# Kernel tuning notes

Measured on AMD Instinct MI355X. Metric: run time of the kernel, lower is better.

## Reference

```python
import jax, jax.numpy as jnp
import numpy as np
from jax import lax

L, H, NUM_CONVS, KSIZE = 8192, 128, 4, 7
EPS = 1e-5


def _pos_encoding(length, dim, dtype):
    pos = jnp.arange(length, dtype=jnp.float32)[:, None]
    i = jnp.arange(dim, dtype=jnp.float32)[None, :]
    angle = pos / jnp.power(10000.0, (2.0 * jnp.floor(i / 2.0)) / dim)
    pe = jnp.where((jnp.arange(dim) % 2 == 0)[None, :], jnp.sin(angle), jnp.cos(angle))
    return pe.astype(dtype)


def _layer_norm(x):
    mu = jnp.mean(x, axis=-1, keepdims=True)
    var = jnp.mean(jnp.square(x - mu), axis=-1, keepdims=True)
    return (x - mu) * lax.rsqrt(var + EPS)


def _conv1d_same(x, w, b):
    # x: [L, H]; w: [H_out, H_in, K]; b: [H_out]. SAME padding over sequence.
    lhs = x.T[None]  # [1, H, L]
    out = lax.conv_general_dilated(lhs, w, window_strides=(1,), padding='SAME',
                                   dimension_numbers=('NCH', 'OIH', 'NCH'))
    return (out[0] + b[:, None]).T  # [L, H]


def setup_inputs() -> dict:
    key = jax.random.key(0)
    ks = jax.random.split(key, 12)
    s = 0.02
    return {
        'x': jax.random.normal(ks[0], (L, H), jnp.float32),
        'conv_w': jax.random.normal(ks[1], (NUM_CONVS, H, H, KSIZE), jnp.float32) * s,
        'conv_b': jax.random.normal(ks[2], (NUM_CONVS, H), jnp.float32) * s,
        'Wq': jax.random.normal(ks[3], (H, H), jnp.float32) * s,
        'bq': jax.random.normal(ks[4], (H,), jnp.float32) * s,
        'Wk': jax.random.normal(ks[5], (H, H), jnp.float32) * s,
        'bk': jax.random.normal(ks[6], (H,), jnp.float32) * s,
        'Wv': jax.random.normal(ks[7], (H, H), jnp.float32) * s,
        'bv': jax.random.normal(ks[8], (H,), jnp.float32) * s,
        'Wff': jax.random.normal(ks[9], (H, H), jnp.float32) * s,
        'bff': jax.random.normal(ks[10], (H,), jnp.float32) * s,
    }


def reference(x, conv_w, conv_b, Wq, bq, Wk, bk, Wv, bv, Wff, bff):
    h = x + _pos_encoding(x.shape[0], x.shape[1], x.dtype)
    # conv stack: LN -> conv -> residual, repeated num_convs times
    for i in range(NUM_CONVS):
        residual = h
        h = _conv1d_same(_layer_norm(h), conv_w[i], conv_b[i]) + residual
    # self-attention (single-head as written in the source)
    residual = h
    n = _layer_norm(h)
    q = n @ Wq.T + bq
    k = n @ Wk.T + bk
    v = n @ Wv.T + bv
    scale = 1.0 / jnp.sqrt(jnp.asarray(H, h.dtype))
    attn = jax.nn.softmax((q @ k.T) * scale, axis=-1)  # [L, L]
    h = attn @ v + residual
    # feed-forward
    residual = h
    h = jax.nn.relu(_layer_norm(h) @ Wff.T + bff) + residual
    return h
```

## Files before the change

### kernel.cpp

```cpp
#include <hip/hip_runtime.h>

#define LL 8192
#define HH 128

typedef __attribute__((ext_vector_type(8))) short short8v;
typedef __attribute__((ext_vector_type(4))) short short4v;
typedef __attribute__((ext_vector_type(4))) float f32x4;

__device__ inline short f2bf(float f) {
    union { float f; unsigned u; } x; x.f = f;
    unsigned r = (x.u + 0x7fffu + ((x.u >> 16) & 1u)) >> 16;
    return (short)r;
}
__device__ inline float bf2f(short s) {
    union { unsigned u; float f; } x; x.u = ((unsigned)(unsigned short)s) << 16;
    return x.f;
}

__global__ __launch_bounds__(256) void repack_conv_wb(const float* __restrict__ w,
                                                      short* __restrict__ wkb) {
    int idx = blockIdx.x * 256 + threadIdx.x;
    int k = idx % 7;
    int t = idx / 7;
    int i = t % HH; t /= HH;
    int o = t % HH;
    int lay = t / HH;
    wkb[((lay * 7 + k) * HH + o) * HH + i] = f2bf(w[idx]);
}

__global__ __launch_bounds__(256) void repack_qkv_wb(const float* __restrict__ Wq,
                                                     const float* __restrict__ Wk,
                                                     const float* __restrict__ Wv,
                                                     const float* __restrict__ bq,
                                                     const float* __restrict__ bk,
                                                     const float* __restrict__ bv,
                                                     short* __restrict__ wqkvb,
                                                     float* __restrict__ b3) {
    const float qs = 0.08838834764831845f;
    int idx = blockIdx.x * 256 + threadIdx.x;
    if (idx < 3 * 16384) {
        int t = idx >> 14, r = idx & 16383;
        float v = (t == 0) ? Wq[r] * qs : (t == 1) ? Wk[r] : Wv[r];
        wqkvb[idx] = f2bf(v);
    } else if (idx < 3 * 16384 + 384) {
        int j = idx - 3 * 16384;
        b3[j] = (j < 128) ? bq[j] * qs : (j < 256) ? bk[j - 128] : bv[j - 256];
    }
}

__global__ __launch_bounds__(256) void repack_ff_wb(const float* __restrict__ Wff,
                                                    short* __restrict__ wffb) {
    int idx = blockIdx.x * 256 + threadIdx.x;
    wffb[idx] = f2bf(Wff[idx]);
}

template <bool POS>
__global__ __launch_bounds__(256) void conv_ln_kernel(const float* __restrict__ hin,
                                                      const short* __restrict__ wkb,
                                                      const float* __restrict__ bias,
                                                      float* __restrict__ hout) {
    __shared__ float sF[22][132];
    __shared__ short sA[22][136];
    int tid = threadIdx.x;
    int w = tid >> 6, lane = tid & 63;
    int l15 = lane & 15, quad = lane >> 4;
    int m0 = blockIdx.x * 16;

    for (int idx = tid; idx < 22 * 32; idx += 256) {
        int r = idx >> 5, c4 = (idx & 31) << 2;
        int gl = m0 - 3 + r;
        float4 val = make_float4(0.f, 0.f, 0.f, 0.f);
        if (gl >= 0 && gl < LL) {
            val = *(const float4*)&hin[gl * HH + c4];
            if (POS) {
#pragma unroll
                for (int j = 0; j < 4; j++) {
                    int i = c4 + j;
                    float e = (float)(i & ~1) / 128.f;
                    float ang = (float)gl / powf(10000.f, e);
                    float pe = (i & 1) ? cosf(ang) : sinf(ang);
                    ((float*)&val)[j] += pe;
                }
            }
        }
        *(float4*)&sF[r][c4] = val;
    }
    __syncthreads();
#pragma unroll
    for (int rr = 0; rr < 6; rr++) {
        int row = rr * 4 + w;
        if (row < 22) {
            float2 xv = *(const float2*)&sF[row][lane * 2];
            float s = xv.x + xv.y, s2 = xv.x * xv.x + xv.y * xv.y;
#pragma unroll
            for (int off = 32; off >= 1; off >>= 1) {
                s  += __shfl_xor(s,  off, 64);
                s2 += __shfl_xor(s2, off, 64);
            }
            float mu = s * (1.f / 128.f);
            float var = s2 * (1.f / 128.f) - mu * mu;
            float rstd = rsqrtf(var + 1e-5f);
            unsigned lo = (unsigned short)f2bf((xv.x - mu) * rstd);
            unsigned hi = (unsigned short)f2bf((xv.y - mu) * rstd);
            ((unsigned*)&sA[row][0])[lane] = lo | (hi << 16);
        }
    }
    __syncthreads();
    int c0 = w * 32;
    f32x4 acc0 = (f32x4)(0.f), acc1 = (f32x4)(0.f);
    for (int k = 0; k < 7; k++) {
        const short* b0 = wkb + (k * HH + c0 + l15) * HH;
        const short* b1 = b0 + 16 * HH;
#pragma unroll
        for (int ks = 0; ks < 4; ks++) {
            short8v af = *(const short8v*)&sA[l15 + k][ks * 32 + quad * 8];
            short8v bf0 = *(const short8v*)&b0[ks * 32 + quad * 8];
            short8v bf1 = *(const short8v*)&b1[ks * 32 + quad * 8];
            acc0 = __builtin_amdgcn_mfma_f32_16x16x32_bf16(af, bf0, acc0, 0, 0, 0);
            acc1 = __builtin_amdgcn_mfma_f32_16x16x32_bf16(af, bf1, acc1, 0, 0, 0);
        }
    }
    float bb0 = bias[c0 + l15], bb1 = bias[c0 + 16 + l15];
#pragma unroll
    for (int r = 0; r < 4; r++) {
        int lr = quad * 4 + r;
        hout[(m0 + lr) * HH + c0 + l15]      = sF[lr + 3][c0 + l15]      + acc0[r] + bb0;
        hout[(m0 + lr) * HH + c0 + 16 + l15] = sF[lr + 3][c0 + 16 + l15] + acc1[r] + bb1;
    }
}

__global__ __launch_bounds__(256) void qkv_kernel(const float* __restrict__ hin,
                                                  const short* __restrict__ wqkvb,
                                                  const float* __restrict__ b3,
                                                  short* __restrict__ qb,
                                                  short* __restrict__ kb,
                                                  short* __restrict__ vt) {
    __shared__ float sF[16][132];
    __shared__ short sA[16][136];
    __shared__ short sT[4][32][17];
    int tid = threadIdx.x;
    int w = tid >> 6, lane = tid & 63;
    int l15 = lane & 15, quad = lane >> 4;
    int m0 = blockIdx.x * 16;

    for (int idx = tid; idx < 16 * 32; idx += 256) {
        int r = idx >> 5, c4 = (idx & 31) << 2;
        *(float4*)&sF[r][c4] = *(const float4*)&hin[(m0 + r) * HH + c4];
    }
    __syncthreads();
#pragma unroll
    for (int rr = 0; rr < 4; rr++) {
        int row = rr * 4 + w;
        float2 xv = *(const float2*)&sF[row][lane * 2];
        float s = xv.x + xv.y, s2 = xv.x * xv.x + xv.y * xv.y;
#pragma unroll
        for (int off = 32; off >= 1; off >>= 1) {
            s  += __shfl_xor(s,  off, 64);
            s2 += __shfl_xor(s2, off, 64);
        }
        float mu = s * (1.f / 128.f);
        float var = s2 * (1.f / 128.f) - mu * mu;
        float rstd = rsqrtf(var + 1e-5f);
        unsigned lo = (unsigned short)f2bf((xv.x - mu) * rstd);
        unsigned hi = (unsigned short)f2bf((xv.y - mu) * rstd);
        ((unsigned*)&sA[row][0])[lane] = lo | (hi << 16);
    }
    __syncthreads();

    short8v af[4];
#pragma unroll
    for (int ks = 0; ks < 4; ks++)
        af[ks] = *(const short8v*)&sA[l15][ks * 32 + quad * 8];
    int c0 = w * 32;

    for (int t = 0; t < 3; t++) {
        f32x4 acc0 = (f32x4)(0.f), acc1 = (f32x4)(0.f);
        const short* b0 = wqkvb + (t * 128 + c0 + l15) * HH;
        const short* b1 = b0 + 16 * HH;
#pragma unroll
        for (int ks = 0; ks < 4; ks++) {
            short8v bf0 = *(const short8v*)&b0[ks * 32 + quad * 8];
            short8v bf1 = *(const short8v*)&b1[ks * 32 + quad * 8];
            acc0 = __builtin_amdgcn_mfma_f32_16x16x32_bf16(af[ks], bf0, acc0, 0, 0, 0);
            acc1 = __builtin_amdgcn_mfma_f32_16x16x32_bf16(af[ks], bf1, acc1, 0, 0, 0);
        }
        float bb0 = b3[t * 128 + c0 + l15], bb1 = b3[t * 128 + c0 + 16 + l15];
        if (t < 2) {
            short* o = (t == 0) ? qb : kb;
#pragma unroll
            for (int r = 0; r < 4; r++) {
                int lr = m0 + quad * 4 + r;
                o[lr * HH + c0 + l15]      = f2bf(acc0[r] + bb0);
                o[lr * HH + c0 + 16 + l15] = f2bf(acc1[r] + bb1);
            }
        } else {
#pragma unroll
            for (int r = 0; r < 4; r++) {
                sT[w][l15][quad * 4 + r]      = f2bf(acc0[r] + bb0);
                sT[w][16 + l15][quad * 4 + r] = f2bf(acc1[r] + bb1);
            }
            asm volatile("s_waitcnt lgkmcnt(0)" ::: "memory");
#pragma unroll
            for (int cc = 0; cc < 8; cc++) {
                int col = cc * 4 + quad;
                vt[(c0 + col) * LL + m0 + l15] = sT[w][col][l15];
            }
        }
    }
}

#define NSPLIT 8
#define SEGROWS (LL / NSPLIT)
#define FBN 64

__global__ __launch_bounds__(256, 2) void flash_mfma_kernel(const short* __restrict__ qs,
                                                            const short* __restrict__ ksrc,
                                                            const short* __restrict__ vsrc,
                                                            short* __restrict__ PO,
                                                            float* __restrict__ Pl) {
    __shared__ short sK[16 * 64 * 8];
    __shared__ short sV[16 * 64 * 8];
    __shared__ short sP[4][32][88];

    const int tid = threadIdx.x;
    const int w = tid >> 6, lane = tid & 63;
    const int l15 = lane & 15, quad = lane >> 4;
    const int m0 = blockIdx.x * 128;
    const int seg = blockIdx.y;
    const int jbeg = seg * SEGROWS;

    const int knt_base = 0;
    const int vdt_base = (w >> 1);
    const int vks2 = w & 1;

    short8v qf[2][4];
#pragma unroll
    for (int mt = 0; mt < 2; mt++)
#pragma unroll
        for (int ks = 0; ks < 4; ks++)
            qf[mt][ks] = *(const short8v*)&qs[(m0 + w * 32 + mt * 16 + l15) * HH + ks * 32 + quad * 8];

    float l_r[2][4] = {{0.f, 0.f, 0.f, 0.f}, {0.f, 0.f, 0.f, 0.f}};
    f32x4 o_acc[2][8];
#pragma unroll
    for (int mt = 0; mt < 2; mt++)
#pragma unroll
        for (int dt = 0; dt < 8; dt++) o_acc[mt][dt] = (f32x4)(0.f);

    short8v kr[4], vr[4];
#pragma unroll
    for (int r = 0; r < 4; r++) {
        kr[r] = *(const short8v*)&ksrc[(jbeg + r * 16 + l15) * HH + w * 32 + quad * 8];
        vr[r] = *(const short8v*)&vsrc[((2 * r + vdt_base) * 16 + l15) * LL + jbeg + vks2 * 32 + quad * 8];
    }

    for (int c = 0; c < SEGROWS / FBN; c++) {
        const int j0 = jbeg + c * FBN;
        __syncthreads();
#pragma unroll
        for (int r = 0; r < 4; r++) {
            *(short8v*)&sK[((w + 4 * r) * 64 + lane) * 8] = kr[r];
            *(short8v*)&sV[((w + 4 * r) * 64 + lane) * 8] = vr[r];
        }
        __syncthreads();
        if (c + 1 < SEGROWS / FBN) {
            const int j1 = j0 + FBN;
#pragma unroll
            for (int r = 0; r < 4; r++) {
                kr[r] = *(const short8v*)&ksrc[(j1 + r * 16 + l15) * HH + w * 32 + quad * 8];
                vr[r] = *(const short8v*)&vsrc[((2 * r + vdt_base) * 16 + l15) * LL + j1 + vks2 * 32 + quad * 8];
            }
        }
        f32x4 s_acc[2][4];
#pragma unroll
        for (int mt = 0; mt < 2; mt++)
#pragma unroll
            for (int nt = 0; nt < 4; nt++) s_acc[mt][nt] = (f32x4)(0.f);
#pragma unroll
        for (int nt = 0; nt < 4; nt++)
#pragma unroll
            for (int ks = 0; ks < 4; ks++) {
                short8v kf = *(const short8v*)&sK[((nt * 4 + ks) * 64 + lane) * 8];
                s_acc[0][nt] = __builtin_amdgcn_mfma_f32_16x16x32_bf16(qf[0][ks], kf, s_acc[0][nt], 0, 0, 0);
                s_acc[1][nt] = __builtin_amdgcn_mfma_f32_16x16x32_bf16(qf[1][ks], kf, s_acc[1][nt], 0, 0, 0);
            }
#pragma unroll
        for (int mt = 0; mt < 2; mt++)
#pragma unroll
            for (int nt = 0; nt < 4; nt++)
#pragma unroll
                for (int r = 0; r < 4; r++) {
                    float p = __expf(fminf(s_acc[mt][nt][r], 30.f));
                    l_r[mt][r] += p;
                    sP[w][mt * 16 + quad * 4 + r][nt * 16 + l15] = f2bf(p);
                }
        asm volatile("s_waitcnt lgkmcnt(0)" ::: "memory");
#pragma unroll
        for (int ks2 = 0; ks2 < 2; ks2++) {
            short8v pf0 = *(const short8v*)&sP[w][l15][ks2 * 32 + quad * 8];
            short8v pf1 = *(const short8v*)&sP[w][16 + l15][ks2 * 32 + quad * 8];
#pragma unroll
            for (int dt = 0; dt < 8; dt++) {
                short8v vf = *(const short8v*)&sV[((dt * 2 + ks2) * 64 + lane) * 8];
                o_acc[0][dt] = __builtin_amdgcn_mfma_f32_16x16x32_bf16(pf0, vf, o_acc[0][dt], 0, 0, 0);
                o_acc[1][dt] = __builtin_amdgcn_mfma_f32_16x16x32_bf16(pf1, vf, o_acc[1][dt], 0, 0, 0);
            }
        }
    }
#pragma unroll
    for (int mt = 0; mt < 2; mt++)
#pragma unroll
        for (int r = 0; r < 4; r++) {
            float v = l_r[mt][r];
            v += __shfl_xor(v, 1, 64);
            v += __shfl_xor(v, 2, 64);
            v += __shfl_xor(v, 4, 64);
            v += __shfl_xor(v, 8, 64);
            if (l15 == 0)
                Pl[seg * LL + m0 + w * 32 + mt * 16 + quad * 4 + r] = v;
        }
#pragma unroll
    for (int mt = 0; mt < 2; mt++)
#pragma unroll
        for (int dt = 0; dt < 8; dt++)
#pragma unroll
            for (int r = 0; r < 4; r++)
                PO[(size_t)seg * LL * HH + (m0 + w * 32 + mt * 16 + quad * 4 + r) * HH + dt * 16 + l15] =
                    f2bf(o_acc[mt][dt][r]);
}

__global__ __launch_bounds__(256) void ff_kernel(const float* __restrict__ hin,
                                                 const short* __restrict__ PO,
                                                 const float* __restrict__ Pl,
                                                 const short* __restrict__ wffb,
                                                 const float* __restrict__ bff,
                                                 float* __restrict__ out) {
    __shared__ float sF[16][132];
    __shared__ short sA[16][136];
    __shared__ float sLi[16];
    int tid = threadIdx.x;
    int w = tid >> 6, lane = tid & 63;
    int l15 = lane & 15, quad = lane >> 4;
    int m0 = blockIdx.x * 16;

    if (tid < 16) {
        float s = 0.f;
#pragma unroll
        for (int seg = 0; seg < NSPLIT; seg++) s += Pl[seg * LL + m0 + tid];
        sLi[tid] = 1.f / s;
    }
    __syncthreads();
    for (int idx = tid; idx < 16 * 32; idx += 256) {
        int r = idx >> 5, c4 = (idx & 31) << 2;
        float4 hv = *(const float4*)&hin[(m0 + r) * HH + c4];
        float s0 = 0.f, s1 = 0.f, s2 = 0.f, s3 = 0.f;
#pragma unroll
        for (int seg = 0; seg < NSPLIT; seg++) {
            short4v pv = *(const short4v*)&PO[(size_t)seg * LL * HH + (m0 + r) * HH + c4];
            s0 += bf2f(pv[0]); s1 += bf2f(pv[1]); s2 += bf2f(pv[2]); s3 += bf2f(pv[3]);
        }
        float li = sLi[r];
        float4 val = make_float4(hv.x + s0 * li, hv.y + s1 * li, hv.z + s2 * li, hv.w + s3 * li);
        *(float4*)&sF[r][c4] = val;
    }
    __syncthreads();
#pragma unroll
    for (int rr = 0; rr < 4; rr++) {
        int row = rr * 4 + w;
        float2 xv = *(const float2*)&sF[row][lane * 2];
        float s = xv.x + xv.y, s2 = xv.x * xv.x + xv.y * xv.y;
#pragma unroll
        for (int off = 32; off >= 1; off >>= 1) {
            s  += __shfl_xor(s,  off, 64);
            s2 += __shfl_xor(s2, off, 64);
        }
        float mu = s * (1.f / 128.f);
        float var = s2 * (1.f / 128.f) - mu * mu;
        float rstd = rsqrtf(var + 1e-5f);
        unsigned lo = (unsigned short)f2bf((xv.x - mu) * rstd);
        unsigned hi = (unsigned short)f2bf((xv.y - mu) * rstd);
        ((unsigned*)&sA[row][0])[lane] = lo | (hi << 16);
    }
    __syncthreads();
    int c0 = w * 32;
    f32x4 acc0 = (f32x4)(0.f), acc1 = (f32x4)(0.f);
    const short* b0 = wffb + (c0 + l15) * HH;
    const short* b1 = b0 + 16 * HH;
#pragma unroll
    for (int ks = 0; ks < 4; ks++) {
        short8v af = *(const short8v*)&sA[l15][ks * 32 + quad * 8];
        short8v bf0 = *(const short8v*)&b0[ks * 32 + quad * 8];
        short8v bf1 = *(const short8v*)&b1[ks * 32 + quad * 8];
        acc0 = __builtin_amdgcn_mfma_f32_16x16x32_bf16(af, bf0, acc0, 0, 0, 0);
        acc1 = __builtin_amdgcn_mfma_f32_16x16x32_bf16(af, bf1, acc1, 0, 0, 0);
    }
    float bb0 = bff[c0 + l15], bb1 = bff[c0 + 16 + l15];
#pragma unroll
    for (int r = 0; r < 4; r++) {
        int lr = quad * 4 + r;
        float z0 = fmaxf(acc0[r] + bb0, 0.f) + sF[lr][c0 + l15];
        float z1 = fmaxf(acc1[r] + bb1, 0.f) + sF[lr][c0 + 16 + l15];
        out[(m0 + lr) * HH + c0 + l15]      = z0;
        out[(m0 + lr) * HH + c0 + 16 + l15] = z1;
    }
}

extern "C" void kernel_launch(void* const* d_in, const int* in_sizes, int n_in,
                              void* d_out, int out_size, void* d_ws, size_t ws_size,
                              hipStream_t stream) {
    const float* x      = (const float*)d_in[0];
    const float* conv_w = (const float*)d_in[1];
    const float* conv_b = (const float*)d_in[2];
    const float* Wq = (const float*)d_in[3];
    const float* bq = (const float*)d_in[4];
    const float* Wk = (const float*)d_in[5];
    const float* bk = (const float*)d_in[6];
    const float* Wv = (const float*)d_in[7];
    const float* bv = (const float*)d_in[8];
    const float* Wff = (const float*)d_in[9];
    const float* bff = (const float*)d_in[10];
    float* out = (float*)d_out;

    char* ws = (char*)d_ws;
    const size_t MB = 1u << 20;
    float* hB    = (float*)(ws);
    short* qb    = (short*)(ws + 4 * MB);
    short* kb    = (short*)(ws + 6 * MB);
    short* vt    = (short*)(ws + 8 * MB);
    float* Pl    = (float*)(ws + 10 * MB);
    short* wffb  = (short*)(ws + 10 * MB + 262144);
    float* b3    = (float*)(ws + 10 * MB + 294912);
    short* PO    = (short*)(ws + 10 * MB + 524288);
    float* hA    = (float*)(ws + 10 * MB + 524288);
    short* wkb   = (short*)(ws + 14 * MB + 524288);
    short* wqkvb = (short*)(ws + 15 * MB + 524288);

    repack_conv_wb<<<1792, 256, 0, stream>>>(conv_w, wkb);
    repack_qkv_wb<<<194, 256, 0, stream>>>(Wq, Wk, Wv, bq, bk, bv, wqkvb, b3);
    repack_ff_wb<<<64, 256, 0, stream>>>(Wff, wffb);

    const int KW = 7 * HH * HH;
    conv_ln_kernel<true ><<<LL / 16, 256, 0, stream>>>(x,  wkb + 0 * KW, conv_b + 0 * HH, hA);
    conv_ln_kernel<false><<<LL / 16, 256, 0, stream>>>(hA, wkb + 1 * KW, conv_b + 1 * HH, hB);
    conv_ln_kernel<false><<<LL / 16, 256, 0, stream>>>(hB, wkb + 2 * KW, conv_b + 2 * HH, hA);
    conv_ln_kernel<false><<<LL / 16, 256, 0, stream>>>(hA, wkb + 3 * KW, conv_b + 3 * HH, hB);

    qkv_kernel<<<LL / 16, 256, 0, stream>>>(hB, wqkvb, b3, qb, kb, vt);

    flash_mfma_kernel<<<dim3(LL / 128, NSPLIT), 256, 0, stream>>>(qb, kb, vt, PO, Pl);

    ff_kernel<<<LL / 16, 256, 0, stream>>>(hB, PO, Pl, wffb, bff, out);
}
```

Measured before the change: 222.0 us.

## Fuse four conv layers and QKV into one halo-recompute kernel, widen attention split

All four LayerNorm+conv residual layers and the QKV projection now run in one kernel. Each block keeps a 48-row window (16 output rows plus 16-row halos) in shared memory across layers, so the intermediate activations no longer round-trip through global memory between launches. The price is about three times the conv MFMA work per output row. The three weight-repack kernels are merged into one launch. When the workspace is large enough, the flash-attention KV split goes from 8 to 16 segments, and P is converted to bf16 by truncation instead of round-to-nearest, which slightly changes numerics.

```diff
diff --git a/kernel.cpp b/kernel.cpp
--- a/kernel.cpp
+++ b/kernel.cpp
@@ -17,161 +17,155 @@
     return x.f;
 }
 
-__global__ __launch_bounds__(256) void repack_conv_wb(const float* __restrict__ w,
-                                                      short* __restrict__ wkb) {
-    int idx = blockIdx.x * 256 + threadIdx.x;
-    int k = idx % 7;
-    int t = idx / 7;
-    int i = t % HH; t /= HH;
-    int o = t % HH;
-    int lay = t / HH;
-    wkb[((lay * 7 + k) * HH + o) * HH + i] = f2bf(w[idx]);
-}
-
-__global__ __launch_bounds__(256) void repack_qkv_wb(const float* __restrict__ Wq,
-                                                     const float* __restrict__ Wk,
-                                                     const float* __restrict__ Wv,
-                                                     const float* __restrict__ bq,
-                                                     const float* __restrict__ bk,
-                                                     const float* __restrict__ bv,
-                                                     short* __restrict__ wqkvb,
-                                                     float* __restrict__ b3) {
+__device__ inline unsigned ln_pack(const float* rowF, int lane) {
+    float2 xv = *(const float2*)&rowF[lane * 2];
+    float s = xv.x + xv.y, s2 = xv.x * xv.x + xv.y * xv.y;
+#pragma unroll
+    for (int off = 32; off >= 1; off >>= 1) {
+        s  += __shfl_xor(s,  off, 64);
+        s2 += __shfl_xor(s2, off, 64);
+    }
+    float mu = s * (1.f / 128.f);
+    float var = s2 * (1.f / 128.f) - mu * mu;
+    float rstd = rsqrtf(var + 1e-5f);
+    unsigned lo = (unsigned short)f2bf((xv.x - mu) * rstd);
+    unsigned hi = (unsigned short)f2bf((xv.y - mu) * rstd);
+    return lo | (hi << 16);
+}
+
+__global__ __launch_bounds__(256) void repack_all(const float* __restrict__ w,
+                                                  const float* __restrict__ Wq,
+                                                  const float* __restrict__ Wk,
+                                                  const float* __restrict__ Wv,
+                                                  const float* __restrict__ bq,
+                                                  const float* __restrict__ bk,
+                                                  const float* __restrict__ bv,
+                                                  const float* __restrict__ Wff,
+                                                  short* __restrict__ wkb,
+                                                  short* __restrict__ wqkvb,
+                                                  float* __restrict__ b3,
+                                                  short* __restrict__ wffb) {
     const float qs = 0.08838834764831845f;
     int idx = blockIdx.x * 256 + threadIdx.x;
-    if (idx < 3 * 16384) {
-        int t = idx >> 14, r = idx & 16383;
-        float v = (t == 0) ? Wq[r] * qs : (t == 1) ? Wk[r] : Wv[r];
-        wqkvb[idx] = f2bf(v);
-    } else if (idx < 3 * 16384 + 384) {
-        int j = idx - 3 * 16384;
-        b3[j] = (j < 128) ? bq[j] * qs : (j < 256) ? bk[j - 128] : bv[j - 256];
-    }
-}
-
-__global__ __launch_bounds__(256) void repack_ff_wb(const float* __restrict__ Wff,
-                                                    short* __restrict__ wffb) {
-    int idx = blockIdx.x * 256 + threadIdx.x;
-    wffb[idx] = f2bf(Wff[idx]);
-}
-
-template <bool POS>
-__global__ __launch_bounds__(256) void conv_ln_kernel(const float* __restrict__ hin,
-                                                      const short* __restrict__ wkb,
-                                                      const float* __restrict__ bias,
-                                                      float* __restrict__ hout) {
-    __shared__ float sF[22][132];
-    __shared__ short sA[22][136];
-    int tid = threadIdx.x;
-    int w = tid >> 6, lane = tid & 63;
-    int l15 = lane & 15, quad = lane >> 4;
-    int m0 = blockIdx.x * 16;
-
-    for (int idx = tid; idx < 22 * 32; idx += 256) {
-        int r = idx >> 5, c4 = (idx & 31) << 2;
-        int gl = m0 - 3 + r;
-        float4 val = make_float4(0.f, 0.f, 0.f, 0.f);
-        if (gl >= 0 && gl < LL) {
-            val = *(const float4*)&hin[gl * HH + c4];
-            if (POS) {
-#pragma unroll
-                for (int j = 0; j < 4; j++) {
-                    int i = c4 + j;
-                    float e = (float)(i & ~1) / 128.f;
-                    float ang = (float)gl / powf(10000.f, e);
-                    float pe = (i & 1) ? cosf(ang) : sinf(ang);
-                    ((float*)&val)[j] += pe;
-                }
-            }
-        }
-        *(float4*)&sF[r][c4] = val;
-    }
-    __syncthreads();
-#pragma unroll
-    for (int rr = 0; rr < 6; rr++) {
-        int row = rr * 4 + w;
-        if (row < 22) {
-            float2 xv = *(const float2*)&sF[row][lane * 2];
-            float s = xv.x + xv.y, s2 = xv.x * xv.x + xv.y * xv.y;
-#pragma unroll
-            for (int off = 32; off >= 1; off >>= 1) {
-                s  += __shfl_xor(s,  off, 64);
-                s2 += __shfl_xor(s2, off, 64);
-            }
-            float mu = s * (1.f / 128.f);
-            float var = s2 * (1.f / 128.f) - mu * mu;
-            float rstd = rsqrtf(var + 1e-5f);
-            unsigned lo = (unsigned short)f2bf((xv.x - mu) * rstd);
-            unsigned hi = (unsigned short)f2bf((xv.y - mu) * rstd);
-            ((unsigned*)&sA[row][0])[lane] = lo | (hi << 16);
-        }
-    }
-    __syncthreads();
-    int c0 = w * 32;
-    f32x4 acc0 = (f32x4)(0.f), acc1 = (f32x4)(0.f);
-    for (int k = 0; k < 7; k++) {
-        const short* b0 = wkb + (k * HH + c0 + l15) * HH;
-        const short* b1 = b0 + 16 * HH;
-#pragma unroll
-        for (int ks = 0; ks < 4; ks++) {
-            short8v af = *(const short8v*)&sA[l15 + k][ks * 32 + quad * 8];
-            short8v bf0 = *(const short8v*)&b0[ks * 32 + quad * 8];
-            short8v bf1 = *(const short8v*)&b1[ks * 32 + quad * 8];
-            acc0 = __builtin_amdgcn_mfma_f32_16x16x32_bf16(af, bf0, acc0, 0, 0, 0);
-            acc1 = __builtin_amdgcn_mfma_f32_16x16x32_bf16(af, bf1, acc1, 0, 0, 0);
-        }
-    }
-    float bb0 = bias[c0 + l15], bb1 = bias[c0 + 16 + l15];
-#pragma unroll
-    for (int r = 0; r < 4; r++) {
-        int lr = quad * 4 + r;
-        hout[(m0 + lr) * HH + c0 + l15]      = sF[lr + 3][c0 + l15]      + acc0[r] + bb0;
-        hout[(m0 + lr) * HH + c0 + 16 + l15] = sF[lr + 3][c0 + 16 + l15] + acc1[r] + bb1;
-    }
-}
-
-__global__ __launch_bounds__(256) void qkv_kernel(const float* __restrict__ hin,
-                                                  const short* __restrict__ wqkvb,
-                                                  const float* __restrict__ b3,
-                                                  short* __restrict__ qb,
-                                                  short* __restrict__ kb,
-                                                  short* __restrict__ vt) {
-    __shared__ float sF[16][132];
-    __shared__ short sA[16][136];
+    if (idx < 458752) {
+        int k = idx % 7;
+        int t = idx / 7;
+        int i = t % HH; t /= HH;
+        int o = t % HH;
+        int lay = t / HH;
+        wkb[((lay * 7 + k) * HH + o) * HH + i] = f2bf(w[idx]);
+    } else {
+        int j = idx - 458752;
+        if (j < 49152) {
+            int t = j >> 14, r = j & 16383;
+            float v = (t == 0) ? Wq[r] * qs : (t == 1) ? Wk[r] : Wv[r];
+            wqkvb[j] = f2bf(v);
+        } else if (j < 49536) {
+            int jj = j - 49152;
+            b3[jj] = (jj < 128) ? bq[jj] * qs : (jj < 256) ? bk[jj - 128] : bv[jj - 256];
+        } else if (j < 65920) {
+            int jj = j - 49536;
+            wffb[jj] = f2bf(Wff[jj]);
+        }
+    }
+}
+
+__global__ __launch_bounds__(256) void conv4qkv_kernel(const float* __restrict__ x,
+                                                       const short* __restrict__ wkb,
+                                                       const float* __restrict__ conv_b,
+                                                       const short* __restrict__ wqkvb,
+                                                       const float* __restrict__ b3,
+                                                       float* __restrict__ hB,
+                                                       short* __restrict__ qb,
+                                                       short* __restrict__ kb,
+                                                       short* __restrict__ vt) {
+    __shared__ float sF[48][132];
+    __shared__ short sA[54][136];
     __shared__ short sT[4][32][17];
     int tid = threadIdx.x;
     int w = tid >> 6, lane = tid & 63;
     int l15 = lane & 15, quad = lane >> 4;
     int m0 = blockIdx.x * 16;
-
+    int c0 = w * 32;
+
+    for (int idx = tid; idx < 48 * 32; idx += 256) {
+        int r = idx >> 5, c4 = (idx & 31) << 2;
+        int g = m0 - 16 + r;
+        float4 val = make_float4(0.f, 0.f, 0.f, 0.f);
+        if (g >= 0 && g < LL) {
+            val = *(const float4*)&x[g * HH + c4];
+#pragma unroll
+            for (int j = 0; j < 4; j++) {
+                int i = c4 + j;
+                float e = (float)(i & ~1) / 128.f;
+                float ang = (float)g / powf(10000.f, e);
+                float pe = (i & 1) ? cosf(ang) : sinf(ang);
+                ((float*)&val)[j] += pe;
+            }
+        }
+        *(float4*)&sF[r][c4] = val;
+    }
+    for (int idx = tid; idx < 6 * 68; idx += 256) {
+        int rr = idx / 68, cc = idx % 68;
+        int row = (rr < 3) ? rr : 48 + rr;
+        ((unsigned*)&sA[row][0])[cc] = 0u;
+    }
+
+    for (int lay = 0; lay < 4; lay++) {
+        __syncthreads();
+#pragma unroll
+        for (int rr = 0; rr < 12; rr++) {
+            int row = rr * 4 + w;
+            int g = m0 - 16 + row;
+            unsigned packed = ln_pack(&sF[row][0], lane);
+            if (g < 0 || g >= LL) packed = 0u;
+            ((unsigned*)&sA[row + 3][0])[lane] = packed;
+        }
+        __syncthreads();
+        f32x4 acc[3][2];
+#pragma unroll
+        for (int mt = 0; mt < 3; mt++) { acc[mt][0] = (f32x4)(0.f); acc[mt][1] = (f32x4)(0.f); }
+        const short* wl = wkb + lay * 7 * HH * HH;
+        for (int k = 0; k < 7; k++) {
+            const short* b0 = wl + (k * HH + c0 + l15) * HH;
+            const short* b1 = b0 + 16 * HH;
+#pragma unroll
+            for (int ks = 0; ks < 4; ks++) {
+                short8v bf0 = *(const short8v*)&b0[ks * 32 + quad * 8];
+                short8v bf1 = *(const short8v*)&b1[ks * 32 + quad * 8];
+#pragma unroll
+                for (int mt = 0; mt < 3; mt++) {
+                    short8v af = *(const short8v*)&sA[mt * 16 + l15 + k][ks * 32 + quad * 8];
+                    acc[mt][0] = __builtin_amdgcn_mfma_f32_16x16x32_bf16(af, bf0, acc[mt][0], 0, 0, 0);
+                    acc[mt][1] = __builtin_amdgcn_mfma_f32_16x16x32_bf16(af, bf1, acc[mt][1], 0, 0, 0);
+                }
+            }
+        }
+        float bb0 = conv_b[lay * HH + c0 + l15], bb1 = conv_b[lay * HH + c0 + 16 + l15];
+#pragma unroll
+        for (int mt = 0; mt < 3; mt++)
+#pragma unroll
+            for (int r = 0; r < 4; r++) {
+                int row = mt * 16 + quad * 4 + r;
+                sF[row][c0 + l15]      += acc[mt][0][r] + bb0;
+                sF[row][c0 + 16 + l15] += acc[mt][1][r] + bb1;
+            }
+    }
+    __syncthreads();
     for (int idx = tid; idx < 16 * 32; idx += 256) {
         int r = idx >> 5, c4 = (idx & 31) << 2;
-        *(float4*)&sF[r][c4] = *(const float4*)&hin[(m0 + r) * HH + c4];
-    }
-    __syncthreads();
+        *(float4*)&hB[(m0 + r) * HH + c4] = *(const float4*)&sF[16 + r][c4];
+    }
 #pragma unroll
     for (int rr = 0; rr < 4; rr++) {
         int row = rr * 4 + w;
-        float2 xv = *(const float2*)&sF[row][lane * 2];
-        float s = xv.x + xv.y, s2 = xv.x * xv.x + xv.y * xv.y;
-#pragma unroll
-        for (int off = 32; off >= 1; off >>= 1) {
-            s  += __shfl_xor(s,  off, 64);
-            s2 += __shfl_xor(s2, off, 64);
-        }
-        float mu = s * (1.f / 128.f);
-        float var = s2 * (1.f / 128.f) - mu * mu;
-        float rstd = rsqrtf(var + 1e-5f);
-        unsigned lo = (unsigned short)f2bf((xv.x - mu) * rstd);
-        unsigned hi = (unsigned short)f2bf((xv.y - mu) * rstd);
-        ((unsigned*)&sA[row][0])[lane] = lo | (hi << 16);
+        ((unsigned*)&sA[row][0])[lane] = ln_pack(&sF[16 + row][0], lane);
     }
     __syncthreads();
-
-    short8v af[4];
+    short8v af4[4];
 #pragma unroll
     for (int ks = 0; ks < 4; ks++)
-        af[ks] = *(const short8v*)&sA[l15][ks * 32 + quad * 8];
-    int c0 = w * 32;
+        af4[ks] = *(const short8v*)&sA[l15][ks * 32 + quad * 8];
 
     for (int t = 0; t < 3; t++) {
         f32x4 acc0 = (f32x4)(0.f), acc1 = (f32x4)(0.f);
@@ -181,8 +175,8 @@
         for (int ks = 0; ks < 4; ks++) {
             short8v bf0 = *(const short8v*)&b0[ks * 32 + quad * 8];
             short8v bf1 = *(const short8v*)&b1[ks * 32 + quad * 8];
-            acc0 = __builtin_amdgcn_mfma_f32_16x16x32_bf16(af[ks], bf0, acc0, 0, 0, 0);
-            acc1 = __builtin_amdgcn_mfma_f32_16x16x32_bf16(af[ks], bf1, acc1, 0, 0, 0);
+            acc0 = __builtin_amdgcn_mfma_f32_16x16x32_bf16(af4[ks], bf0, acc0, 0, 0, 0);
+            acc1 = __builtin_amdgcn_mfma_f32_16x16x32_bf16(af4[ks], bf1, acc1, 0, 0, 0);
         }
         float bb0 = b3[t * 128 + c0 + l15], bb1 = b3[t * 128 + c0 + 16 + l15];
         if (t < 2) {
@@ -209,27 +203,26 @@
     }
 }
 
-#define NSPLIT 8
-#define SEGROWS (LL / NSPLIT)
 #define FBN 64
 
 __global__ __launch_bounds__(256, 2) void flash_mfma_kernel(const short* __restrict__ qs,
                                                             const short* __restrict__ ksrc,
                                                             const short* __restrict__ vsrc,
                                                             short* __restrict__ PO,
-                                                            float* __restrict__ Pl) {
+                                                            float* __restrict__ Pl,
+                                                            int segrows) {
     __shared__ short sK[16 * 64 * 8];
     __shared__ short sV[16 * 64 * 8];
-    __shared__ short sP[4][32][88];
+    __shared__ short sP[4][32][72];
 
     const int tid = threadIdx.x;
     const int w = tid >> 6, lane = tid & 63;
     const int l15 = lane & 15, quad = lane >> 4;
     const int m0 = blockIdx.x * 128;
     const int seg = blockIdx.y;
-    const int jbeg = seg * SEGROWS;
-
-    const int knt_base = 0;
+    const int jbeg = seg * segrows;
+    const int nchunk = segrows >> 6;
+
     const int vdt_base = (w >> 1);
     const int vks2 = w & 1;
 
@@ -254,8 +247,7 @@
         vr[r] = *(const short8v*)&vsrc[((2 * r + vdt_base) * 16 + l15) * LL + jbeg + vks2 * 32 + quad * 8];
     }
 
-    for (int c = 0; c < SEGROWS / FBN; c++) {
-        const int j0 = jbeg + c * FBN;
+    for (int c = 0; c < nchunk; c++) {
         __syncthreads();
 #pragma unroll
         for (int r = 0; r < 4; r++) {
@@ -263,8 +255,8 @@
             *(short8v*)&sV[((w + 4 * r) * 64 + lane) * 8] = vr[r];
         }
         __syncthreads();
-        if (c + 1 < SEGROWS / FBN) {
-            const int j1 = j0 + FBN;
+        if (c + 1 < nchunk) {
+            const int j1 = jbeg + (c + 1) * FBN;
 #pragma unroll
             for (int r = 0; r < 4; r++) {
                 kr[r] = *(const short8v*)&ksrc[(j1 + r * 16 + l15) * HH + w * 32 + quad * 8];
@@ -292,7 +284,8 @@
                 for (int r = 0; r < 4; r++) {
                     float p = __expf(fminf(s_acc[mt][nt][r], 30.f));
                     l_r[mt][r] += p;
-                    sP[w][mt * 16 + quad * 4 + r][nt * 16 + l15] = f2bf(p);
+                    union { float f; unsigned u; } cv; cv.f = p;
+                    sP[w][mt * 16 + quad * 4 + r][nt * 16 + l15] = (short)(cv.u >> 16);
                 }
         asm volatile("s_waitcnt lgkmcnt(0)" ::: "memory");
 #pragma unroll
@@ -334,7 +327,8 @@
                                                  const float* __restrict__ Pl,
                                                  const short* __restrict__ wffb,
                                                  const float* __restrict__ bff,
-                                                 float* __restrict__ out) {
+                                                 float* __restrict__ out,
+                                                 int nsplit) {
     __shared__ float sF[16][132];
     __shared__ short sA[16][136];
     __shared__ float sLi[16];
@@ -345,8 +339,7 @@
 
     if (tid < 16) {
         float s = 0.f;
-#pragma unroll
-        for (int seg = 0; seg < NSPLIT; seg++) s += Pl[seg * LL + m0 + tid];
+        for (int seg = 0; seg < nsplit; seg++) s += Pl[seg * LL + m0 + tid];
         sLi[tid] = 1.f / s;
     }
     __syncthreads();
@@ -354,32 +347,19 @@
         int r = idx >> 5, c4 = (idx & 31) << 2;
         float4 hv = *(const float4*)&hin[(m0 + r) * HH + c4];
         float s0 = 0.f, s1 = 0.f, s2 = 0.f, s3 = 0.f;
-#pragma unroll
-        for (int seg = 0; seg < NSPLIT; seg++) {
+        for (int seg = 0; seg < nsplit; seg++) {
             short4v pv = *(const short4v*)&PO[(size_t)seg * LL * HH + (m0 + r) * HH + c4];
             s0 += bf2f(pv[0]); s1 += bf2f(pv[1]); s2 += bf2f(pv[2]); s3 += bf2f(pv[3]);
         }
         float li = sLi[r];
-        float4 val = make_float4(hv.x + s0 * li, hv.y + s1 * li, hv.z + s2 * li, hv.w + s3 * li);
-        *(float4*)&sF[r][c4] = val;
+        *(float4*)&sF[r][c4] = make_float4(hv.x + s0 * li, hv.y + s1 * li,
+                                           hv.z + s2 * li, hv.w + s3 * li);
     }
     __syncthreads();
 #pragma unroll
     for (int rr = 0; rr < 4; rr++) {
         int row = rr * 4 + w;
-        float2 xv = *(const float2*)&sF[row][lane * 2];
-        float s = xv.x + xv.y, s2 = xv.x * xv.x + xv.y * xv.y;
-#pragma unroll
-        for (int off = 32; off >= 1; off >>= 1) {
-            s  += __shfl_xor(s,  off, 64);
-            s2 += __shfl_xor(s2, off, 64);
-        }
-        float mu = s * (1.f / 128.f);
-        float var = s2 * (1.f / 128.f) - mu * mu;
-        float rstd = rsqrtf(var + 1e-5f);
-        unsigned lo = (unsigned short)f2bf((xv.x - mu) * rstd);
-        unsigned hi = (unsigned short)f2bf((xv.y - mu) * rstd);
-        ((unsigned*)&sA[row][0])[lane] = lo | (hi << 16);
+        ((unsigned*)&sA[row][0])[lane] = ln_pack(&sF[row][0], lane);
     }
     __syncthreads();
     int c0 = w * 32;
@@ -398,10 +378,8 @@
 #pragma unroll
     for (int r = 0; r < 4; r++) {
         int lr = quad * 4 + r;
-        float z0 = fmaxf(acc0[r] + bb0, 0.f) + sF[lr][c0 + l15];
-        float z1 = fmaxf(acc1[r] + bb1, 0.f) + sF[lr][c0 + 16 + l15];
-        out[(m0 + lr) * HH + c0 + l15]      = z0;
-        out[(m0 + lr) * HH + c0 + 16 + l15] = z1;
+        out[(m0 + lr) * HH + c0 + l15]      = fmaxf(acc0[r] + bb0, 0.f) + sF[lr][c0 + l15];
+        out[(m0 + lr) * HH + c0 + 16 + l15] = fmaxf(acc1[r] + bb1, 0.f) + sF[lr][c0 + 16 + l15];
     }
 }
 
@@ -423,31 +401,24 @@
 
     char* ws = (char*)d_ws;
     const size_t MB = 1u << 20;
-    float* hB    = (float*)(ws);
-    short* qb    = (short*)(ws + 4 * MB);
-    short* kb    = (short*)(ws + 6 * MB);
-    short* vt    = (short*)(ws + 8 * MB);
-    float* Pl    = (float*)(ws + 10 * MB);
-    short* wffb  = (short*)(ws + 10 * MB + 262144);
-    float* b3    = (float*)(ws + 10 * MB + 294912);
-    short* PO    = (short*)(ws + 10 * MB + 524288);
-    float* hA    = (float*)(ws + 10 * MB + 524288);
-    short* wkb   = (short*)(ws + 14 * MB + 524288);
-    short* wqkvb = (short*)(ws + 15 * MB + 524288);
-
-    repack_conv_wb<<<1792, 256, 0, stream>>>(conv_w, wkb);
-    repack_qkv_wb<<<194, 256, 0, stream>>>(Wq, Wk, Wv, bq, bk, bv, wqkvb, b3);
-    repack_ff_wb<<<64, 256, 0, stream>>>(Wff, wffb);
-
-    const int KW = 7 * HH * HH;
-    conv_ln_kernel<true ><<<LL / 16, 256, 0, stream>>>(x,  wkb + 0 * KW, conv_b + 0 * HH, hA);
-    conv_ln_kernel<false><<<LL / 16, 256, 0, stream>>>(hA, wkb + 1 * KW, conv_b + 1 * HH, hB);
-    conv_ln_kernel<false><<<LL / 16, 256, 0, stream>>>(hB, wkb + 2 * KW, conv_b + 2 * HH, hA);
-    conv_ln_kernel<false><<<LL / 16, 256, 0, stream>>>(hA, wkb + 3 * KW, conv_b + 3 * HH, hB);
-
-    qkv_kernel<<<LL / 16, 256, 0, stream>>>(hB, wqkvb, b3, qb, kb, vt);
-
-    flash_mfma_kernel<<<dim3(LL / 128, NSPLIT), 256, 0, stream>>>(qb, kb, vt, PO, Pl);
-
-    ff_kernel<<<LL / 16, 256, 0, stream>>>(hB, PO, Pl, wffb, bff, out);
-}
+    float* hB   = (float*)(ws);
+    short* qb   = (short*)(ws + 4 * MB);
+    short* kb   = (short*)(ws + 6 * MB);
+    short* vt   = (short*)(ws + 8 * MB);
+    float* Pl   = (float*)(ws + 10 * MB);
+    short* wffb = (short*)(ws + 10 * MB + 524288);
+    short* PO   = (short*)(ws + 10 * MB + 524288 + 32768);
+    short* wkb   = (short*)(ws + 16 * MB);
+    short* wqkvb = (short*)(ws + 17 * MB);
+    float* b3    = (float*)(ws + 17 * MB + 131072);
+
+    int nsplit = (ws_size >= (size_t)44 * MB) ? 16 : 8;
+    int segrows = LL / nsplit;
+
+    repack_all<<<2050, 256, 0, stream>>>(conv_w, Wq, Wk, Wv, bq, bk, bv, Wff,
+                                         wkb, wqkvb, b3, wffb);
+    conv4qkv_kernel<<<LL / 16, 256, 0, stream>>>(x, wkb, conv_b, wqkvb, b3,
+                                                 hB, qb, kb, vt);
+    flash_mfma_kernel<<<dim3(LL / 128, nsplit), 256, 0, stream>>>(qb, kb, vt, PO, Pl, segrows);
+    ff_kernel<<<LL / 16, 256, 0, stream>>>(hB, PO, Pl, wffb, bff, out, nsplit);
+}
```

Result: faster. 217.3 us (-2.1%).
